# Kernel tuning notes

Hardware: AMD Instinct MI355X
Metric: run time of the kernel (lower is better)

Reference implementation:

```python
import jax, jax.numpy as jnp
import numpy as np

B, N, E, ATT, TT, IT = 32, 5000, 500, 50, 4, 24
TEMP = 0.5

def leaky(x):
    return jnp.where(x > 0, x, 0.1 * x)

def ln(x, g, b, eps=1e-5):
    m = jnp.mean(x, axis=-1, keepdims=True)
    v = jnp.mean((x - m) ** 2, axis=-1, keepdims=True)
    return (x - m) * jax.lax.rsqrt(v + eps) * g + b

def setup_inputs() -> dict:
    key = jax.random.key(0)
    ks = jax.random.split(key, 16)
    s = 0.05
    return {
        'positive_sample': jax.random.randint(ks[0], (B, 3), 0, N),
        'ent_text_emb': jax.random.normal(ks[1], (N, TT, 384), jnp.float32),
        'ent_img_emb': jax.random.normal(ks[2], (N, IT, 383), jnp.float32),
        'entity_embedding': jax.random.normal(ks[3], (N, E), jnp.float32) * s,
        'relation_embedding': jax.random.normal(ks[4], (N, E), jnp.float32) * s,
        'W_text': jax.random.normal(ks[5], (ATT, 384), jnp.float32) * s,
        'b_text': jnp.zeros((ATT,), jnp.float32),
        'W_img': jax.random.normal(ks[6], (ATT, 383), jnp.float32) * s,
        'b_img': jnp.zeros((ATT,), jnp.float32),
        'W_tproj': jax.random.normal(ks[7], (ATT, ATT * IT), jnp.float32) * s,
        'b_tproj': jnp.zeros((ATT,), jnp.float32),
        'W_iproj': jax.random.normal(ks[8], (ATT, ATT * TT), jnp.float32) * s,
        'b_iproj': jnp.zeros((ATT,), jnp.float32),
        'W_rel1': jax.random.normal(ks[9], (IT * TT, E), jnp.float32) * s,
        'b_rel1': jnp.zeros((IT * TT,), jnp.float32),
        'W_rel2': jax.random.normal(ks[10], (IT * TT, E), jnp.float32) * s,
        'b_rel2': jnp.zeros((IT * TT,), jnp.float32),
        'W1': jax.random.normal(ks[11], (100, 2 * E), jnp.float32) * s,
        'b1': jnp.zeros((100,), jnp.float32),
        'W3': jax.random.normal(ks[12], (E, 100), jnp.float32) * s,
        'b3': jnp.zeros((E,), jnp.float32),
        'ln_g': jnp.ones((ATT,), jnp.float32),
        'ln_b': jnp.zeros((ATT,), jnp.float32),
    }

def _cos_sim(X, p):
    # X [B,N,d], p [B,d]; denominators are detached as in the torch code
    num = jnp.einsum('bnd,bd->bn', X, p)
    den = jnp.linalg.norm(X, axis=2) * jnp.linalg.norm(p, axis=1)[:, None]
    return num / (jax.lax.stop_gradient(den) + 1e-10)

def reference(positive_sample, ent_text_emb, ent_img_emb, entity_embedding,
              relation_embedding, W_text, b_text, W_img, b_img, W_tproj, b_tproj,
              W_iproj, b_iproj, W_rel1, b_rel1, W_rel2, b_rel2, W1, b1, W3, b3,
              ln_g, ln_b):
    rel = relation_embedding[positive_sample[:, 1]]              # [B,E]
    text_emb = leaky(jnp.einsum('ntf,df->ntd', ent_text_emb, W_text) + b_text)  # [N,4,50]
    img_emb = leaky(jnp.einsum('nif,df->nid', ent_img_emb, W_img) + b_img)      # [N,24,50]
    cross = jnp.einsum('nid,ntd->nit', img_emb, text_emb)        # [N,24,4]

    # image branch: softmax over img tokens, plus relation-gated path
    img_att = jnp.einsum('nti,nid->ntd', jax.nn.softmax(cross.transpose(0, 2, 1), axis=2), img_emb)  # [N,4,50]
    rg_i = jax.nn.sigmoid(rel @ W_rel1.T + b_rel1).reshape(B, IT, TT)           # [B,24,4]
    gated_i = rg_i[:, None] * cross[None]                                        # [B,N,24,4]
    img_att_rg = jnp.einsum('bnit,nid->bntd', gated_i, img_emb)                  # [B,N,4,50]
    img_att_all = ln(img_att_rg, ln_g, ln_b) + ln(img_att, ln_g, ln_b)[None]
    img_att_all = img_att_all.reshape(B, N, TT * ATT) @ W_iproj.T + b_iproj      # [B,N,50]

    # text branch: softmax over text tokens, plus relation-gated path
    text_att = jnp.einsum('nit,ntd->nid', jax.nn.softmax(cross, axis=2), text_emb)  # [N,24,50]
    rg_t = jax.nn.sigmoid(rel @ W_rel2.T + b_rel2).reshape(B, IT, TT)
    gated_t = rg_t[:, None] * cross[None]                                        # [B,N,24,4]
    text_att_rg = jnp.einsum('bnit,ntd->bnid', gated_t, text_emb)                # [B,N,24,50]
    text_att_all = ln(text_att_rg, ln_g, ln_b) + ln(text_att, ln_g, ln_b)[None]
    text_att_all = text_att_all.reshape(B, N, IT * ATT) @ W_tproj.T + b_tproj    # [B,N,50]

    # structural gate on KGE entity embeddings (split W1 to avoid concat)
    h = leaky(entity_embedding @ W1[:, :E].T[None].squeeze(0).T.T  # placeholder removed below
              ) if False else None
    h = leaky((entity_embedding @ W1[:, :E].T)[None] + (rel @ W1[:, E:].T)[:, None] + b1)  # [B,N,100]
    gate = jax.nn.sigmoid(h @ W3.T + b3)                                         # [B,N,E]
    t_att = entity_embedding[None] * gate                                        # [B,N,E]

    pos_idx = positive_sample[:, 2]  # tail-batch
    bi = jnp.arange(B)
    pos_img = img_att_all[bi, pos_idx]    # [B,50]
    pos_text = text_att_all[bi, pos_idx]  # [B,50]
    pos_t = t_att[bi, pos_idx]            # [B,E]

    simil_img = _cos_sim(img_att_all, pos_img)
    simil_text = _cos_sim(text_att_all, pos_text)
    simil_t = _cos_sim(t_att, pos_t)

    out = (jax.nn.softmax(simil_t / TEMP, axis=1)
           + jax.nn.softmax(simil_img / TEMP, axis=1)
           + jax.nn.softmax(simil_text / TEMP, axis=1))
    return (out, simil_img, simil_text, simil_t)
```

## Files before the change

### kernel.cpp

```cpp
#include <hip/hip_runtime.h>
#include <math.h>

#define BB 32
#define NN 5000
#define EE 500
#define AT 50
#define TTT 4
#define ITT 24
#define FT 384
#define FI 383
#define KH 100
#define BN (BB*NN)

__device__ __forceinline__ float leaky(float x){ return x > 0.f ? x : 0.1f*x; }
__device__ __forceinline__ float sigm(float x){ return 1.f/(1.f+__expf(-x)); }

enum : size_t {
  O_WTT = 0,
  O_WIT = 19968,
  O_WIP = 39936,
  O_WTP = 50336,
  O_W1T = 112736,
  O_W3T = 162736,
  O_SIP = 212736,
  O_STP = 212944,
  O_CBI = 214192,
  O_CBT = 214244,
  O_RGI = 214296,
  O_RGT = 217368,
  O_RB  = 220440,
  O_A   = 223640,
  O_PT  = 723640,
  O_PTN = 739640,
  O_PIM = 739672,
  O_PIMN= 741336,
  O_PTX = 741368,
  O_PTXN= 743032,
  O_MR  = 743064,
  O_SR  = 743160,
  O_EMB = 743256,
};

__global__ void k_prep(const float* Wt, const float* Wi, const float* Wip, const float* Wtp,
                       const float* W1, const float* W3, const float* g, const float* lb,
                       const float* bip, const float* btp, float* ws){
  (void)W1;
  int id = blockIdx.x*256 + threadIdx.x;
  if (id < 19968){ int f=id/52, d=id%52; ws[O_WTT+id] = (d<50)? Wt[d*FT+f] : 0.f; return; }
  id -= 19968;
  if (id < 19968){ int f=id/52, d=id%52; ws[O_WIT+id] = (f<383 && d<50)? Wi[d*FI+f] : 0.f; return; }
  id -= 19968;
  if (id < 10400){
    int m=id>>2, c=id&3; int d=m%50, r=m/50; int q=r%13, t=r/13; int o=q*4+c;
    ws[O_WIP+id] = (o<50)? Wip[o*200+t*50+d]*g[o] : 0.f; return; }
  id -= 10400;
  if (id < 62400){
    int m=id>>2, c=id&3; int d=m%50, r=m/50; int q=r%13, i=r/13; int o=q*4+c;
    ws[O_WTP+id] = (o<50)? Wtp[o*1200+i*50+d]*g[o] : 0.f; return; }
  id -= 62400;
  if (id < 50000){ int k=id/500, e=id%500; ws[O_W3T+id] = W3[e*100+k]; return; }
  id -= 50000;
  if (id < 208){ int t=id/52, o=id%52; float s=0;
                 if (o<50) for(int d=0;d<50;d++) s += Wip[o*200+t*50+d]*g[d];
                 ws[O_SIP+id]=s; return; }
  id -= 208;
  if (id < 1248){ int i=id/52, o=id%52; float s=0;
                  if (o<50) for(int d=0;d<50;d++) s += Wtp[o*1200+i*50+d]*g[d];
                  ws[O_STP+id]=s; return; }
  id -= 1248;
  if (id < 52){ int o=id; float s=0;
                if (o<50){ for(int j=0;j<200;j++) s += lb[j%50]*Wip[o*200+j]; s=2.f*s+bip[o]; }
                ws[O_CBI+o]=s; return; }
  id -= 52;
  if (id < 52){ int o=id; float s=0;
                if (o<50){ for(int j=0;j<1200;j++) s += lb[j%50]*Wtp[o*1200+j]; s=2.f*s+btp[o]; }
                ws[O_CBT+o]=s; return; }
}

__global__ void k_rel(const int* ps, const float* rele, const float* Wr1, const float* br1,
                      const float* Wr2, const float* br2, const float* W1, float* ws){
  __shared__ float relL[EE];
  int b = blockIdx.x;
  int r = ps[b*3+1];
  for (int e=threadIdx.x; e<EE; e+=256) relL[e] = rele[(size_t)r*EE+e];
  __syncthreads();
  for (int j=threadIdx.x; j<292; j+=256){
    if (j<96){
      float a=br1[j]; const float* w=&Wr1[j*EE];
      for(int e=0;e<EE;e++) a+=relL[e]*w[e];
      ws[O_RGI+b*96+j]=sigm(a);
    } else if (j<192){
      int jj=j-96; float a=br2[jj]; const float* w=&Wr2[jj*EE];
      for(int e=0;e<EE;e++) a+=relL[e]*w[e];
      ws[O_RGT+b*96+jj]=sigm(a);
    } else {
      int k=j-192; float a=0; const float* w=&W1[k*1000+500];
      for(int e=0;e<EE;e++) a+=relL[e]*w[e];
      ws[O_RB+b*100+k]=a;
    }
  }
}

__global__ void k_A(const float* ent, const float* W1, float* ws){
  __shared__ __align__(16) float entL[8*EE];
  int n0 = blockIdx.x*8;
  for (int idx=threadIdx.x; idx<1000; idx+=256)
    *(float4*)&entL[idx*4] = *(const float4*)&ent[(size_t)n0*EE + idx*4];
  __syncthreads();
  for (int idx=threadIdx.x; idx<800; idx+=256){
    int k=idx>>3, rr=idx&7;
    const float4* el=(const float4*)&entL[rr*EE];
    const float4* wr=(const float4*)&W1[(size_t)k*1000];
    float s=0;
    for (int e4=0;e4<125;e4++){
      float4 a=el[e4], w=wr[e4];
      s += a.x*w.x + a.y*w.y + a.z*w.z + a.w*w.w;
    }
    ws[O_A + (size_t)k*NN + (n0+rr)] = s;
  }
}

__global__ void k_pos(const int* ps, const float* ent, const float* b1, const float* b3, float* ws){
  __shared__ float hL[KH];
  __shared__ float red[4];
  int b=blockIdx.x; int n=ps[b*3+2]; int tid=threadIdx.x;
  if (tid<KH) hL[tid] = leaky(ws[O_A+(size_t)tid*NN+n] + ws[O_RB+b*100+tid] + b1[tid]);
  __syncthreads();
  const float* w3t=&ws[O_W3T];
  float sq=0;
  for (int e=tid; e<EE; e+=256){
    float a=b3[e];
    for (int k=0;k<KH;k++) a += hL[k]*w3t[k*500+e];
    float gg=sigm(a); float ta=ent[(size_t)n*EE+e]*gg;
    ws[O_PT+b*500+e]=ta; sq+=ta*ta;
  }
  for (int off=1; off<64; off<<=1) sq += __shfl_xor(sq, off);
  if ((tid&63)==0) red[tid>>6]=sq;
  __syncthreads();
  if (tid==0) ws[O_PTN+b] = sqrtf(red[0]+red[1]+red[2]+red[3]);
}

__global__ __launch_bounds__(256) void k_emb2(const float* __restrict__ X,
                                              const float* __restrict__ Wp,
                                              const float* __restrict__ bias,
                                              float* __restrict__ emb,
                                              int R, int F, int rowsPerN, int rowOff,
                                              int xstride){
  __shared__ __align__(16) float part[4][64][52];
  int tid = threadIdx.x;
  int lane = tid & 63;
  int w = __builtin_amdgcn_readfirstlane(tid >> 6);
  int row = blockIdx.x*64 + lane;
  int fq = (F + 3) >> 2;
  int f0 = w*fq;
  int f1 = min(F, f0+fq);
  float4 acc[13];
  #pragma unroll
  for (int c=0;c<13;c++) acc[c]=make_float4(0,0,0,0);
  if (row < R){
    const float* xr = X + (size_t)row*xstride;
    for (int f=f0; f<f1; ++f){
      float x = xr[f];
      const float4* wr = (const float4*)(Wp + (size_t)f*52);
      #pragma unroll
      for (int c=0;c<13;++c){
        float4 wv=wr[c];
        acc[c].x+=x*wv.x; acc[c].y+=x*wv.y; acc[c].z+=x*wv.z; acc[c].w+=x*wv.w;
      }
    }
  }
  #pragma unroll
  for (int c=0;c<13;c++) *(float4*)&part[w][lane][c*4] = acc[c];
  __syncthreads();
  for (int g=tid; g<832; g+=256){
    int r = g/13, q = g-r*13;
    int row2 = blockIdx.x*64 + r;
    if (row2 < R){
      float4 s0 = *(const float4*)&part[0][r][q*4];
      float4 s1 = *(const float4*)&part[1][r][q*4];
      float4 s2 = *(const float4*)&part[2][r][q*4];
      float4 s3 = *(const float4*)&part[3][r][q*4];
      float4 v;
      v.x = leaky(s0.x+s1.x+s2.x+s3.x + bias[q*4+0]);
      v.y = leaky(s0.y+s1.y+s2.y+s3.y + bias[q*4+1]);
      v.z = (q<12)? leaky(s0.z+s1.z+s2.z+s3.z + bias[q*4+2]) : 0.f;
      v.w = (q<12)? leaky(s0.w+s1.w+s2.w+s3.w + bias[q*4+3]) : 0.f;
      int n = row2 / rowsPerN, rr = row2 % rowsPerN;
      *(float4*)&emb[(size_t)n*1456 + (size_t)(rowOff+rr)*52 + q*4] = v;
    }
  }
}

__global__ __launch_bounds__(256) void k_main(const int* ps, float* ws, float* out, int mode){
  __shared__ __align__(16) float teie[1456];
  __shared__ __align__(16) float Pm[120*52];
  __shared__ __align__(16) float Um[120*32];
  __shared__ __align__(16) float Gi[576];
  __shared__ __align__(16) float crs[96];
  __shared__ __align__(16) float aimg[96], atxt[96];
  __shared__ __align__(16) float part1[96], part2[96];
  __shared__ __align__(16) float aU[120];
  __shared__ float Gts[16], mimg[24], mtxt[4];
  __shared__ float muA1[4], muA2[24];
  __shared__ float accD1[32], accN1[32], accD2[32], accN2[32];

  int tid = threadIdx.x;
  int bstar = blockIdx.x;
  int n = mode ? ps[bstar*3+2] : blockIdx.x;

  const float* embn = &ws[O_EMB + (size_t)n*1456];
  for (int j=tid; j<364; j+=256) *(float4*)&teie[j*4] = *(const float4*)&embn[j*4];
  if (tid<32){ accD1[tid]=0.f; accN1[tid]=0.f; accD2[tid]=0.f; accN2[tid]=0.f; }
  __syncthreads();

  for (int it=tid; it<716; it+=256){
    if (it<576){
      int i=it/24, j=it%24;
      const float4* a=(const float4*)&teie[(4+i)*52];
      const float4* b=(const float4*)&teie[(4+j)*52];
      float s=0;
      #pragma unroll
      for(int d=0;d<13;d++){ float4 x=a[d], y=b[d]; s+=x.x*y.x+x.y*y.y+x.z*y.z+x.w*y.w; }
      Gi[it]=s;
    } else if (it<672){
      int c=it-576; int i=c>>2, t=c&3;
      const float4* a=(const float4*)&teie[(4+i)*52];
      const float4* b=(const float4*)&teie[t*52];
      float s=0;
      #pragma unroll
      for(int d=0;d<13;d++){ float4 x=a[d], y=b[d]; s+=x.x*y.x+x.y*y.y+x.z*y.z+x.w*y.w; }
      crs[c]=s;
    } else if (it<688){
      int c=it-672; int t=c>>2, u=c&3;
      const float4* a=(const float4*)&teie[t*52];
      const float4* b=(const float4*)&teie[u*52];
      float s=0;
      #pragma unroll
      for(int d=0;d<13;d++){ float4 x=a[d], y=b[d]; s+=x.x*y.x+x.y*y.y+x.z*y.z+x.w*y.w; }
      Gts[c]=s;
    } else if (it<712){
      int i=it-688;
      const float4* a=(const float4*)&teie[(4+i)*52];
      float s=0;
      #pragma unroll
      for(int d=0;d<13;d++){ float4 x=a[d]; s+=x.x+x.y+x.z+x.w; }
      mimg[i]=s*0.02f;
    } else {
      int t=it-712;
      const float4* a=(const float4*)&teie[t*52];
      float s=0;
      #pragma unroll
      for(int d=0;d<13;d++){ float4 x=a[d]; s+=x.x+x.y+x.z+x.w; }
      mtxt[t]=s*0.02f;
    }
  }
  __syncthreads();

  if (tid<4){
    int t=tid;
    float mx=-1e30f; for(int i=0;i<24;i++) mx=fmaxf(mx,crs[i*4+t]);
    float ex[24]; float s=0;
    for(int i=0;i<24;i++){ ex[i]=__expf(crs[i*4+t]-mx); s+=ex[i]; }
    float inv=1.f/s; float mu=0;
    for(int i=0;i<24;i++){ float a=ex[i]*inv; aimg[i*4+t]=a; mu+=a*mimg[i]; }
    muA1[t]=mu;
  } else if (tid>=64 && tid<88){
    int i=tid-64;
    float mx=-1e30f; for(int t=0;t<4;t++) mx=fmaxf(mx,crs[i*4+t]);
    float ex[4]; float s=0;
    for(int t=0;t<4;t++){ ex[t]=__expf(crs[i*4+t]-mx); s+=ex[t]; }
    float inv=1.f/s; float mu=0;
    for(int t=0;t<4;t++){ float a=ex[t]*inv; atxt[i*4+t]=a; mu+=a*mtxt[t]; }
    muA2[i]=mu;
  }
  __syncthreads();

  if (tid<208){
    int ig=tid&3, r=tid>>2, q=r%13, t=r/13;
    const float* wb = &ws[O_WIP + (size_t)(t*13+q)*200];
    const float* eb = &teie[(4+ig*6)*52];
    float4 acc[6];
    #pragma unroll
    for (int l=0;l<6;l++) acc[l]=make_float4(0,0,0,0);
    for (int dc=0; dc<12; ++dc){
      float e[6][4];
      #pragma unroll
      for (int l=0;l<6;l++){
        float4 v=*(const float4*)&eb[l*52+dc*4];
        e[l][0]=v.x; e[l][1]=v.y; e[l][2]=v.z; e[l][3]=v.w;
      }
      #pragma unroll
      for (int dd=0; dd<4; ++dd){
        float4 w=*(const float4*)&wb[(dc*4+dd)*4];
        #pragma unroll
        for (int l=0;l<6;l++){
          acc[l].x+=e[l][dd]*w.x; acc[l].y+=e[l][dd]*w.y;
          acc[l].z+=e[l][dd]*w.z; acc[l].w+=e[l][dd]*w.w;
        }
      }
    }
    #pragma unroll
    for (int d=48; d<50; ++d){
      float4 w=*(const float4*)&wb[d*4];
      #pragma unroll
      for (int l=0;l<6;l++){
        float ee=eb[l*52+d];
        acc[l].x+=ee*w.x; acc[l].y+=ee*w.y; acc[l].z+=ee*w.z; acc[l].w+=ee*w.w;
      }
    }
    #pragma unroll
    for (int l=0;l<6;l++) *(float4*)&Pm[(t*24+ig*6+l)*52 + q*4]=acc[l];
  } else {
    for (int c=tid-208; c<244; c+=48){
      if (c<96){
        int i=c>>2, t=c&3;
        float s=0; for(int j=0;j<24;j++) s+=Gi[i*24+j]*aimg[j*4+t];
        part1[c]=aimg[c]*s;
      } else if (c<192){
        int cc=c-96; int t=cc&3;
        float s=0; for(int u=0;u<4;u++) s+=Gts[t*4+u]*atxt[(cc&~3)+u];
        part2[cc]=atxt[cc]*s;
      } else {
        int j=c-192;
        *(float4*)&Pm[96*52+j*4] = *(const float4*)&ws[O_SIP+j*4];
      }
    }
  }
  __syncthreads();

  if (tid<128){
    int b=tid&31, t=tid>>5;
    float w1r[24];
    #pragma unroll
    for(int i=0;i<24;i++) w1r[i]=ws[O_RGI+b*96+i*4+t]*crs[i*4+t];
    float mu=0;
    #pragma unroll
    for(int i=0;i<24;i++) mu+=w1r[i]*mimg[i];
    float q=0;
    #pragma unroll
    for(int i=0;i<24;i++){
      const float4* gr=(const float4*)&Gi[i*24];
      float s=0;
      #pragma unroll
      for(int j4=0;j4<6;j4++){
        float4 g=gr[j4];
        s+=g.x*w1r[j4*4]+g.y*w1r[j4*4+1]+g.z*w1r[j4*4+2]+g.w*w1r[j4*4+3];
      }
      q+=w1r[i]*s;
    }
    float inv=rsqrtf(q*0.02f-mu*mu+1e-5f);
    #pragma unroll
    for(int i=0;i<24;i++) Um[(t*24+i)*32+b]=inv*w1r[i];
    Um[(96+t)*32+b]=-inv*mu;
  } else if (tid<228){
    int z=tid-128;
    int t=(z<96)? (z/24) : (z-96);
    float q=0; for(int i=0;i<24;i++) q+=part1[i*4+t];
    float inv=rsqrtf(q*0.02f-muA1[t]*muA1[t]+1e-5f);
    aU[z]=(z<96)? inv*aimg[(z%24)*4+t] : -inv*muA1[t];
  }
  __syncthreads();

  if (tid<104){
    int bg=tid/13, q=tid-bg*13;
    float4 a0=make_float4(0,0,0,0), a1=make_float4(0,0,0,0);
    float4 a2=make_float4(0,0,0,0), a3=make_float4(0,0,0,0);
    for (int z=0; z<100; ++z){
      float az=aU[z];
      float4 u=*(const float4*)&Um[z*32+bg*4];
      float4 p=*(const float4*)&Pm[z*52+q*4];
      float u0=u.x+az, u1=u.y+az, u2=u.z+az, u3=u.w+az;
      a0.x+=u0*p.x; a0.y+=u0*p.y; a0.z+=u0*p.z; a0.w+=u0*p.w;
      a1.x+=u1*p.x; a1.y+=u1*p.y; a1.z+=u1*p.z; a1.w+=u1*p.w;
      a2.x+=u2*p.x; a2.y+=u2*p.y; a2.z+=u2*p.z; a2.w+=u2*p.w;
      a3.x+=u3*p.x; a3.y+=u3*p.y; a3.z+=u3*p.z; a3.w+=u3*p.w;
    }
    float4 cb=*(const float4*)&ws[O_CBI+q*4];
    a0.x+=cb.x; a0.y+=cb.y; a0.z+=cb.z; a0.w+=cb.w;
    a1.x+=cb.x; a1.y+=cb.y; a1.z+=cb.z; a1.w+=cb.w;
    a2.x+=cb.x; a2.y+=cb.y; a2.z+=cb.z; a2.w+=cb.w;
    a3.x+=cb.x; a3.y+=cb.y; a3.z+=cb.z; a3.w+=cb.w;
    float n0=a0.x*a0.x+a0.y*a0.y+a0.z*a0.z+a0.w*a0.w;
    float n1=a1.x*a1.x+a1.y*a1.y+a1.z*a1.z+a1.w*a1.w;
    float n2=a2.x*a2.x+a2.y*a2.y+a2.z*a2.z+a2.w*a2.w;
    float n3=a3.x*a3.x+a3.y*a3.y+a3.z*a3.z+a3.w*a3.w;
    int b0=bg*4;
    if (!mode){
      const float* PV=&ws[O_PIM];
      float4 p0=*(const float4*)&PV[(b0+0)*52+q*4];
      float4 p1=*(const float4*)&PV[(b0+1)*52+q*4];
      float4 p2=*(const float4*)&PV[(b0+2)*52+q*4];
      float4 p3=*(const float4*)&PV[(b0+3)*52+q*4];
      atomicAdd(&accD1[b0+0], a0.x*p0.x+a0.y*p0.y+a0.z*p0.z+a0.w*p0.w);
      atomicAdd(&accD1[b0+1], a1.x*p1.x+a1.y*p1.y+a1.z*p1.z+a1.w*p1.w);
      atomicAdd(&accD1[b0+2], a2.x*p2.x+a2.y*p2.y+a2.z*p2.z+a2.w*p2.w);
      atomicAdd(&accD1[b0+3], a3.x*p3.x+a3.y*p3.y+a3.z*p3.z+a3.w*p3.w);
      atomicAdd(&accN1[b0+0],n0); atomicAdd(&accN1[b0+1],n1);
      atomicAdd(&accN1[b0+2],n2); atomicAdd(&accN1[b0+3],n3);
    } else {
      atomicAdd(&accN1[b0+0],n0); atomicAdd(&accN1[b0+1],n1);
      atomicAdd(&accN1[b0+2],n2); atomicAdd(&accN1[b0+3],n3);
      if ((bstar>>2)==bg){
        int bl=bstar&3;
        float4 sel = (bl==0)? a0 : (bl==1)? a1 : (bl==2)? a2 : a3;
        *(float4*)&ws[O_PIM+(size_t)bstar*52+q*4]=sel;
      }
    }
  }
  __syncthreads();

  if (!mode){
    if (tid<32)
      out[(size_t)BN + (size_t)tid*NN + n] = accD1[tid]/(sqrtf(accN1[tid])*ws[O_PIMN+tid]+1e-10f);
  } else {
    if (tid==0) ws[O_PIMN+bstar]=sqrtf(accN1[bstar]);
  }
  if (tid<156){
    int q=tid%13, i2=tid/13;
    const float* wbA = &ws[O_WTP + (size_t)((i2*2+0)*13+q)*200];
    const float* wbB = &ws[O_WTP + (size_t)((i2*2+1)*13+q)*200];
    float4 accA[4], accB[4];
    #pragma unroll
    for (int t=0;t<4;t++){ accA[t]=make_float4(0,0,0,0); accB[t]=make_float4(0,0,0,0); }
    for (int dc=0; dc<12; ++dc){
      float e[4][4];
      #pragma unroll
      for (int t=0;t<4;t++){
        float4 v=*(const float4*)&teie[t*52+dc*4];
        e[t][0]=v.x; e[t][1]=v.y; e[t][2]=v.z; e[t][3]=v.w;
      }
      #pragma unroll
      for (int dd=0; dd<4; ++dd){
        float4 wA=*(const float4*)&wbA[(dc*4+dd)*4];
        float4 wB=*(const float4*)&wbB[(dc*4+dd)*4];
        #pragma unroll
        for (int t=0;t<4;t++){
          accA[t].x+=e[t][dd]*wA.x; accA[t].y+=e[t][dd]*wA.y;
          accA[t].z+=e[t][dd]*wA.z; accA[t].w+=e[t][dd]*wA.w;
          accB[t].x+=e[t][dd]*wB.x; accB[t].y+=e[t][dd]*wB.y;
          accB[t].z+=e[t][dd]*wB.z; accB[t].w+=e[t][dd]*wB.w;
        }
      }
    }
    #pragma unroll
    for (int d=48; d<50; ++d){
      float4 wA=*(const float4*)&wbA[d*4];
      float4 wB=*(const float4*)&wbB[d*4];
      #pragma unroll
      for (int t=0;t<4;t++){
        float ee=teie[t*52+d];
        accA[t].x+=ee*wA.x; accA[t].y+=ee*wA.y; accA[t].z+=ee*wA.z; accA[t].w+=ee*wA.w;
        accB[t].x+=ee*wB.x; accB[t].y+=ee*wB.y; accB[t].z+=ee*wB.z; accB[t].w+=ee*wB.w;
      }
    }
    #pragma unroll
    for (int t=0;t<4;t++){
      *(float4*)&Pm[(t*24+i2*2+0)*52 + q*4]=accA[t];
      *(float4*)&Pm[(t*24+i2*2+1)*52 + q*4]=accB[t];
    }
  } else {
    for (int j=tid-156; j<312; j+=100)
      *(float4*)&Pm[96*52+j*4] = *(const float4*)&ws[O_STP+j*4];
  }
  __syncthreads();

  for (int it=tid; it<888; it+=256){
    if (it<768){
      int b=it&31, i=it>>5;
      float w2r[4];
      #pragma unroll
      for(int t=0;t<4;t++) w2r[t]=ws[O_RGT+b*96+i*4+t]*crs[i*4+t];
      float mu=0;
      #pragma unroll
      for(int t=0;t<4;t++) mu+=w2r[t]*mtxt[t];
      float q=0;
      #pragma unroll
      for(int t=0;t<4;t++){
        float s=0;
        #pragma unroll
        for(int u=0;u<4;u++) s+=Gts[t*4+u]*w2r[u];
        q+=w2r[t]*s;
      }
      float inv=rsqrtf(q*0.02f-mu*mu+1e-5f);
      #pragma unroll
      for(int t=0;t<4;t++) Um[(t*24+i)*32+b]=inv*w2r[t];
      Um[(96+i)*32+b]=-inv*mu;
    } else {
      int z=it-768;
      int i=(z<96)? (z%24) : (z-96);
      float q=0; for(int t=0;t<4;t++) q+=part2[i*4+t];
      float inv=rsqrtf(q*0.02f-muA2[i]*muA2[i]+1e-5f);
      aU[z]=(z<96)? inv*atxt[(z%24)*4+(z/24)] : -inv*muA2[i];
    }
  }
  __syncthreads();

  if (tid<104){
    int bg=tid/13, q=tid-bg*13;
    float4 a0=make_float4(0,0,0,0), a1=make_float4(0,0,0,0);
    float4 a2=make_float4(0,0,0,0), a3=make_float4(0,0,0,0);
    for (int z=0; z<120; ++z){
      float az=aU[z];
      float4 u=*(const float4*)&Um[z*32+bg*4];
      float4 p=*(const float4*)&Pm[z*52+q*4];
      float u0=u.x+az, u1=u.y+az, u2=u.z+az, u3=u.w+az;
      a0.x+=u0*p.x; a0.y+=u0*p.y; a0.z+=u0*p.z; a0.w+=u0*p.w;
      a1.x+=u1*p.x; a1.y+=u1*p.y; a1.z+=u1*p.z; a1.w+=u1*p.w;
      a2.x+=u2*p.x; a2.y+=u2*p.y; a2.z+=u2*p.z; a2.w+=u2*p.w;
      a3.x+=u3*p.x; a3.y+=u3*p.y; a3.z+=u3*p.z; a3.w+=u3*p.w;
    }
    float4 cb=*(const float4*)&ws[O_CBT+q*4];
    a0.x+=cb.x; a0.y+=cb.y; a0.z+=cb.z; a0.w+=cb.w;
    a1.x+=cb.x; a1.y+=cb.y; a1.z+=cb.z; a1.w+=cb.w;
    a2.x+=cb.x; a2.y+=cb.y; a2.z+=cb.z; a2.w+=cb.w;
    a3.x+=cb.x; a3.y+=cb.y; a3.z+=cb.z; a3.w+=cb.w;
    float n0=a0.x*a0.x+a0.y*a0.y+a0.z*a0.z+a0.w*a0.w;
    float n1=a1.x*a1.x+a1.y*a1.y+a1.z*a1.z+a1.w*a1.w;
    float n2=a2.x*a2.x+a2.y*a2.y+a2.z*a2.z+a2.w*a2.w;
    float n3=a3.x*a3.x+a3.y*a3.y+a3.z*a3.z+a3.w*a3.w;
    int b0=bg*4;
    if (!mode){
      const float* PV=&ws[O_PTX];
      float4 p0=*(const float4*)&PV[(b0+0)*52+q*4];
      float4 p1=*(const float4*)&PV[(b0+1)*52+q*4];
      float4 p2=*(const float4*)&PV[(b0+2)*52+q*4];
      float4 p3=*(const float4*)&PV[(b0+3)*52+q*4];
      atomicAdd(&accD2[b0+0], a0.x*p0.x+a0.y*p0.y+a0.z*p0.z+a0.w*p0.w);
      atomicAdd(&accD2[b0+1], a1.x*p1.x+a1.y*p1.y+a1.z*p1.z+a1.w*p1.w);
      atomicAdd(&accD2[b0+2], a2.x*p2.x+a2.y*p2.y+a2.z*p2.z+a2.w*p2.w);
      atomicAdd(&accD2[b0+3], a3.x*p3.x+a3.y*p3.y+a3.z*p3.z+a3.w*p3.w);
      atomicAdd(&accN2[b0+0],n0); atomicAdd(&accN2[b0+1],n1);
      atomicAdd(&accN2[b0+2],n2); atomicAdd(&accN2[b0+3],n3);
    } else {
      atomicAdd(&accN2[b0+0],n0); atomicAdd(&accN2[b0+1],n1);
      atomicAdd(&accN2[b0+2],n2); atomicAdd(&accN2[b0+3],n3);
      if ((bstar>>2)==bg){
        int bl=bstar&3;
        float4 sel = (bl==0)? a0 : (bl==1)? a1 : (bl==2)? a2 : a3;
        *(float4*)&ws[O_PTX+(size_t)bstar*52+q*4]=sel;
      }
    }
  }
  __syncthreads();

  if (!mode){
    if (tid<32)
      out[2*(size_t)BN + (size_t)tid*NN + n] = accD2[tid]/(sqrtf(accN2[tid])*ws[O_PTXN+tid]+1e-10f);
  } else {
    if (tid==0) ws[O_PTXN+bstar]=sqrtf(accN2[bstar]);
  }
}

__global__ __launch_bounds__(256) void k_gate(const float* ent, const float* b1, const float* b3,
                                              float* ws, float* out){
  __shared__ __align__(16) float hL[50*68];
  __shared__ __align__(16) float wc[50*128];
  __shared__ __align__(16) float PTb[512];
  __shared__ __align__(16) float b3L[512];
  __shared__ float rbL[KH];

  int tid = threadIdx.x;
  int b   = blockIdx.x & 31;
  int n0  = (blockIdx.x >> 5) * 64;

  for (int j=tid; j<512; j+=256){
    PTb[j] = (j<EE)? ws[O_PT + b*EE + j] : 0.f;
    b3L[j] = (j<EE)? b3[j] : 0.f;
  }
  if (tid < KH) rbL[tid] = ws[O_RB + b*KH + tid] + b1[tid];

  int ej = tid & 31;
  int ni = tid >> 5;

  float pn[8], ps[8];
  #pragma unroll
  for (int r=0;r<8;r++){ pn[r]=0.f; ps[r]=0.f; }

  for (int ec=0; ec<4; ++ec){
    int e0 = ec*128;
    float4 acc[8];
    #pragma unroll
    for (int r=0;r<8;r++) acc[r]=make_float4(0,0,0,0);

    for (int kh=0; kh<2; ++kh){
      __syncthreads();
      for (int idx=tid; idx<1600; idx+=256){
        int k = idx>>5, j4 = idx&31;
        int e = e0 + j4*4;
        float4 v = make_float4(0,0,0,0);
        if (e+3 < EE) v = *(const float4*)&ws[O_W3T + (size_t)(kh*50+k)*EE + e];
        *(float4*)&wc[k*128 + j4*4] = v;
      }
      for (int idx=tid; idx<3200; idx+=256){
        int k = idx>>6, nn = idx&63;
        int n = n0 + nn;
        float v = 0.f;
        if (n < NN) v = leaky(ws[O_A + (size_t)(kh*50+k)*NN + n] + rbL[kh*50+k]);
        hL[k*68 + nn] = v;
      }
      __syncthreads();

      const float4* wp = (const float4*)&wc[ej*4];
      const float4* hp = (const float4*)&hL[ni*8];
      #pragma unroll 2
      for (int k=0;k<50;k++){
        float4 w  = wp[k*32];
        float4 h0 = hp[k*17];
        float4 h1 = hp[k*17 + 1];
        acc[0].x+=h0.x*w.x; acc[0].y+=h0.x*w.y; acc[0].z+=h0.x*w.z; acc[0].w+=h0.x*w.w;
        acc[1].x+=h0.y*w.x; acc[1].y+=h0.y*w.y; acc[1].z+=h0.y*w.z; acc[1].w+=h0.y*w.w;
        acc[2].x+=h0.z*w.x; acc[2].y+=h0.z*w.y; acc[2].z+=h0.z*w.z; acc[2].w+=h0.z*w.w;
        acc[3].x+=h0.w*w.x; acc[3].y+=h0.w*w.y; acc[3].z+=h0.w*w.z; acc[3].w+=h0.w*w.w;
        acc[4].x+=h1.x*w.x; acc[4].y+=h1.x*w.y; acc[4].z+=h1.x*w.z; acc[4].w+=h1.x*w.w;
        acc[5].x+=h1.y*w.x; acc[5].y+=h1.y*w.y; acc[5].z+=h1.y*w.z; acc[5].w+=h1.y*w.w;
        acc[6].x+=h1.z*w.x; acc[6].y+=h1.z*w.y; acc[6].z+=h1.z*w.z; acc[6].w+=h1.z*w.w;
        acc[7].x+=h1.w*w.x; acc[7].y+=h1.w*w.y; acc[7].z+=h1.w*w.z; acc[7].w+=h1.w*w.w;
      }
    }

    {
      int ebase = e0 + ej*4;
      bool ev = (ebase + 3) < EE;
      float4 bb = *(const float4*)&b3L[ebase];
      float4 pt = *(const float4*)&PTb[ebase];
      #pragma unroll
      for (int r=0;r<8;r++){
        int n = n0 + ni*8 + r;
        float4 en = make_float4(0,0,0,0);
        if (ev && n < NN) en = *(const float4*)&ent[(size_t)n*EE + ebase];
        float t0 = en.x * sigm(acc[r].x + bb.x);
        float t1 = en.y * sigm(acc[r].y + bb.y);
        float t2 = en.z * sigm(acc[r].z + bb.z);
        float t3 = en.w * sigm(acc[r].w + bb.w);
        pn[r] += t0*pt.x + t1*pt.y + t2*pt.z + t3*pt.w;
        ps[r] += t0*t0 + t1*t1 + t2*t2 + t3*t3;
      }
    }
  }

  for (int off=1; off<32; off<<=1){
    #pragma unroll
    for (int r=0;r<8;r++){ pn[r]+=__shfl_xor(pn[r],off); ps[r]+=__shfl_xor(ps[r],off); }
  }
  if (ej==0){
    float ptn = ws[O_PTN+b];
    #pragma unroll
    for (int r=0;r<8;r++){
      int n = n0 + ni*8 + r;
      if (n < NN)
        out[3*(size_t)BN + (size_t)b*NN + n] = pn[r]/(sqrtf(ps[r])*ptn + 1e-10f);
    }
  }
}

__global__ void k_smax1(const float* out, float* ws){
  __shared__ float red[4];
  __shared__ float Msh;
  int a=blockIdx.x>>5, b=blockIdx.x&31, tid=threadIdx.x;
  const float* arr=&out[(size_t)(1+a)*BN + (size_t)b*NN];
  float mx=-1e30f;
  for (int i=tid;i<NN;i+=256) mx=fmaxf(mx,arr[i]);
  for (int off=1;off<64;off<<=1) mx=fmaxf(mx,__shfl_xor(mx,off));
  if ((tid&63)==0) red[tid>>6]=mx;
  __syncthreads();
  if (tid==0) Msh=fmaxf(fmaxf(red[0],red[1]),fmaxf(red[2],red[3]));
  __syncthreads();
  float M2=2.f*Msh;
  float s=0;
  for (int i=tid;i<NN;i+=256) s+=__expf(2.f*arr[i]-M2);
  for (int off=1;off<64;off<<=1) s+=__shfl_xor(s,off);
  if ((tid&63)==0) red[tid>>6]=s;
  __syncthreads();
  if (tid==0){ ws[O_MR+a*32+b]=M2; ws[O_SR+a*32+b]=red[0]+red[1]+red[2]+red[3]; }
}

__global__ void k_smax2(float* out, const float* ws){
  int t=blockIdx.x*256+threadIdx.x;
  if (t>=BN) return;
  int b=t/NN;
  float r=0;
  for (int a=0;a<3;a++)
    r += __expf(2.f*out[(size_t)(1+a)*BN+t]-ws[O_MR+a*32+b])/ws[O_SR+a*32+b];
  out[t]=r;
}

extern "C" void kernel_launch(void* const* d_in, const int* in_sizes, int n_in,
                              void* d_out, int out_size, void* d_ws, size_t ws_size,
                              hipStream_t stream){
  (void)in_sizes; (void)n_in; (void)out_size; (void)ws_size;
  const int*   ps  =(const int*)  d_in[0];
  const float* etg =(const float*)d_in[1];
  const float* eig =(const float*)d_in[2];
  const float* ent =(const float*)d_in[3];
  const float* rele=(const float*)d_in[4];
  const float* Wt  =(const float*)d_in[5];
  const float* btx =(const float*)d_in[6];
  const float* Wi  =(const float*)d_in[7];
  const float* bim =(const float*)d_in[8];
  const float* Wtp =(const float*)d_in[9];
  const float* btp =(const float*)d_in[10];
  const float* Wip =(const float*)d_in[11];
  const float* bip =(const float*)d_in[12];
  const float* Wr1 =(const float*)d_in[13];
  const float* br1 =(const float*)d_in[14];
  const float* Wr2 =(const float*)d_in[15];
  const float* br2 =(const float*)d_in[16];
  const float* W1  =(const float*)d_in[17];
  const float* b1  =(const float*)d_in[18];
  const float* W3  =(const float*)d_in[19];
  const float* b3  =(const float*)d_in[20];
  const float* lng =(const float*)d_in[21];
  const float* lnb =(const float*)d_in[22];
  float* ws =(float*)d_ws;
  float* out=(float*)d_out;

  k_prep <<<642,256,0,stream>>>(Wt,Wi,Wip,Wtp,W1,W3,lng,lnb,bip,btp,ws);
  k_rel  <<<32, 256,0,stream>>>(ps,rele,Wr1,br1,Wr2,br2,W1,ws);
  k_A    <<<625,256,0,stream>>>(ent,W1,ws);
  k_pos  <<<32, 256,0,stream>>>(ps,ent,b1,b3,ws);
  k_emb2 <<<313, 256,0,stream>>>(etg,&ws[O_WTT],btx,&ws[O_EMB],20000,FT,4,0,FT);
  k_emb2 <<<1875,256,0,stream>>>(eig,&ws[O_WIT],bim,&ws[O_EMB],120000,FI,24,4,FI);
  k_main <<<32,  256,0,stream>>>(ps,ws,out,1);
  k_main <<<5000,256,0,stream>>>(ps,ws,out,0);
  k_gate <<<32*79,256,0,stream>>>(ent,b1,b3,ws,out);
  k_smax1<<<96, 256,0,stream>>>(out,ws);
  k_smax2<<<625,256,0,stream>>>(out,ws);
}
```

Measured before the change: 1.457 ms.

## Fuse LN coefficient and projection stages using register accumulation and wave shuffles

The image and text attention stages used to write per-batch normalization coefficients into shared matrices (Um, aU), synchronize, and then run a separate small GEMM with shared-memory atomics for the dot products and norms. Now each thread computes its coefficients and multiplies them directly against the Pm rows, keeping a 13-float4 partial output in registers. Partials are combined with xor-shuffle reductions across 4 or 8 lanes, and one lane writes the cosine similarity. This removes several barriers, the shared atomics and some shared memory, at the cost of more registers per thread and redundant Pm reads across lanes.

```diff
diff --git a/kernel.cpp b/kernel.cpp
--- a/kernel.cpp
+++ b/kernel.cpp
@@ -194,15 +194,12 @@
 __global__ __launch_bounds__(256) void k_main(const int* ps, float* ws, float* out, int mode){
   __shared__ __align__(16) float teie[1456];
   __shared__ __align__(16) float Pm[120*52];
-  __shared__ __align__(16) float Um[120*32];
   __shared__ __align__(16) float Gi[576];
   __shared__ __align__(16) float crs[96];
   __shared__ __align__(16) float aimg[96], atxt[96];
   __shared__ __align__(16) float part1[96], part2[96];
-  __shared__ __align__(16) float aU[120];
   __shared__ float Gts[16], mimg[24], mtxt[4];
   __shared__ float muA1[4], muA2[24];
-  __shared__ float accD1[32], accN1[32], accD2[32], accN2[32];
 
   int tid = threadIdx.x;
   int bstar = blockIdx.x;
@@ -210,7 +207,6 @@
 
   const float* embn = &ws[O_EMB + (size_t)n*1456];
   for (int j=tid; j<364; j+=256) *(float4*)&teie[j*4] = *(const float4*)&embn[j*4];
-  if (tid<32){ accD1[tid]=0.f; accN1[tid]=0.f; accD2[tid]=0.f; accN2[tid]=0.f; }
   __syncthreads();
 
   for (int it=tid; it<716; it+=256){
@@ -328,8 +324,9 @@
   }
   __syncthreads();
 
-  if (tid<128){
-    int b=tid&31, t=tid>>5;
+  if (tid < 128){
+    int l = tid & 63, wv = tid >> 6;
+    int b = wv*16 + (l>>2), t = l&3;
     float w1r[24];
     #pragma unroll
     for(int i=0;i<24;i++) w1r[i]=ws[O_RGI+b*96+i*4+t]*crs[i*4+t];
@@ -349,72 +346,66 @@
       q+=w1r[i]*s;
     }
     float inv=rsqrtf(q*0.02f-mu*mu+1e-5f);
-    #pragma unroll
-    for(int i=0;i<24;i++) Um[(t*24+i)*32+b]=inv*w1r[i];
-    Um[(96+t)*32+b]=-inv*mu;
-  } else if (tid<228){
-    int z=tid-128;
-    int t=(z<96)? (z/24) : (z-96);
-    float q=0; for(int i=0;i<24;i++) q+=part1[i*4+t];
-    float inv=rsqrtf(q*0.02f-muA1[t]*muA1[t]+1e-5f);
-    aU[z]=(z<96)? inv*aimg[(z%24)*4+t] : -inv*muA1[t];
-  }
-  __syncthreads();
-
-  if (tid<104){
-    int bg=tid/13, q=tid-bg*13;
-    float4 a0=make_float4(0,0,0,0), a1=make_float4(0,0,0,0);
-    float4 a2=make_float4(0,0,0,0), a3=make_float4(0,0,0,0);
-    for (int z=0; z<100; ++z){
-      float az=aU[z];
-      float4 u=*(const float4*)&Um[z*32+bg*4];
-      float4 p=*(const float4*)&Pm[z*52+q*4];
-      float u0=u.x+az, u1=u.y+az, u2=u.z+az, u3=u.w+az;
-      a0.x+=u0*p.x; a0.y+=u0*p.y; a0.z+=u0*p.z; a0.w+=u0*p.w;
-      a1.x+=u1*p.x; a1.y+=u1*p.y; a1.z+=u1*p.z; a1.w+=u1*p.w;
-      a2.x+=u2*p.x; a2.y+=u2*p.y; a2.z+=u2*p.z; a2.w+=u2*p.w;
-      a3.x+=u3*p.x; a3.y+=u3*p.y; a3.z+=u3*p.z; a3.w+=u3*p.w;
-    }
-    float4 cb=*(const float4*)&ws[O_CBI+q*4];
-    a0.x+=cb.x; a0.y+=cb.y; a0.z+=cb.z; a0.w+=cb.w;
-    a1.x+=cb.x; a1.y+=cb.y; a1.z+=cb.z; a1.w+=cb.w;
-    a2.x+=cb.x; a2.y+=cb.y; a2.z+=cb.z; a2.w+=cb.w;
-    a3.x+=cb.x; a3.y+=cb.y; a3.z+=cb.z; a3.w+=cb.w;
-    float n0=a0.x*a0.x+a0.y*a0.y+a0.z*a0.z+a0.w*a0.w;
-    float n1=a1.x*a1.x+a1.y*a1.y+a1.z*a1.z+a1.w*a1.w;
-    float n2=a2.x*a2.x+a2.y*a2.y+a2.z*a2.z+a2.w*a2.w;
-    float n3=a3.x*a3.x+a3.y*a3.y+a3.z*a3.z+a3.w*a3.w;
-    int b0=bg*4;
-    if (!mode){
-      const float* PV=&ws[O_PIM];
-      float4 p0=*(const float4*)&PV[(b0+0)*52+q*4];
-      float4 p1=*(const float4*)&PV[(b0+1)*52+q*4];
-      float4 p2=*(const float4*)&PV[(b0+2)*52+q*4];
-      float4 p3=*(const float4*)&PV[(b0+3)*52+q*4];
-      atomicAdd(&accD1[b0+0], a0.x*p0.x+a0.y*p0.y+a0.z*p0.z+a0.w*p0.w);
-      atomicAdd(&accD1[b0+1], a1.x*p1.x+a1.y*p1.y+a1.z*p1.z+a1.w*p1.w);
-      atomicAdd(&accD1[b0+2], a2.x*p2.x+a2.y*p2.y+a2.z*p2.z+a2.w*p2.w);
-      atomicAdd(&accD1[b0+3], a3.x*p3.x+a3.y*p3.y+a3.z*p3.z+a3.w*p3.w);
-      atomicAdd(&accN1[b0+0],n0); atomicAdd(&accN1[b0+1],n1);
-      atomicAdd(&accN1[b0+2],n2); atomicAdd(&accN1[b0+3],n3);
-    } else {
-      atomicAdd(&accN1[b0+0],n0); atomicAdd(&accN1[b0+1],n1);
-      atomicAdd(&accN1[b0+2],n2); atomicAdd(&accN1[b0+3],n3);
-      if ((bstar>>2)==bg){
-        int bl=bstar&3;
-        float4 sel = (bl==0)? a0 : (bl==1)? a1 : (bl==2)? a2 : a3;
-        *(float4*)&ws[O_PIM+(size_t)bstar*52+q*4]=sel;
-      }
-    }
-  }
-  __syncthreads();
-
-  if (!mode){
-    if (tid<32)
-      out[(size_t)BN + (size_t)tid*NN + n] = accD1[tid]/(sqrtf(accN1[tid])*ws[O_PIMN+tid]+1e-10f);
-  } else {
-    if (tid==0) ws[O_PIMN+bstar]=sqrtf(accN1[bstar]);
-  }
+    float qa=0;
+    #pragma unroll
+    for(int i=0;i<24;i++) qa+=part1[i*4+t];
+    float invA=rsqrtf(qa*0.02f-muA1[t]*muA1[t]+1e-5f);
+
+    float4 res[13];
+    #pragma unroll
+    for (int c=0;c<13;c++) res[c]=make_float4(0,0,0,0);
+    for (int j=0;j<24;j++){
+      int i = j + t*6; if (i>=24) i-=24;
+      float c = inv*w1r[i] + invA*aimg[i*4+t];
+      const float4* pr=(const float4*)&Pm[(t*24+i)*52];
+      #pragma unroll
+      for (int cc=0;cc<13;cc++){
+        float4 p=pr[cc];
+        res[cc].x+=c*p.x; res[cc].y+=c*p.y; res[cc].z+=c*p.z; res[cc].w+=c*p.w;
+      }
+    }
+    {
+      float cS = -inv*mu - invA*muA1[t];
+      const float4* pr=(const float4*)&Pm[(96+t)*52];
+      #pragma unroll
+      for (int cc=0;cc<13;cc++){
+        float4 p=pr[cc];
+        res[cc].x+=cS*p.x; res[cc].y+=cS*p.y; res[cc].z+=cS*p.z; res[cc].w+=cS*p.w;
+      }
+    }
+    #pragma unroll
+    for (int cc=0;cc<13;cc++){
+      res[cc].x+=__shfl_xor(res[cc].x,1); res[cc].y+=__shfl_xor(res[cc].y,1);
+      res[cc].z+=__shfl_xor(res[cc].z,1); res[cc].w+=__shfl_xor(res[cc].w,1);
+      res[cc].x+=__shfl_xor(res[cc].x,2); res[cc].y+=__shfl_xor(res[cc].y,2);
+      res[cc].z+=__shfl_xor(res[cc].z,2); res[cc].w+=__shfl_xor(res[cc].w,2);
+    }
+    if (t==0){
+      float ni=0;
+      #pragma unroll
+      for (int cc=0;cc<13;cc++){
+        float4 cb=*(const float4*)&ws[O_CBI+cc*4];
+        res[cc].x+=cb.x; res[cc].y+=cb.y; res[cc].z+=cb.z; res[cc].w+=cb.w;
+        ni+=res[cc].x*res[cc].x+res[cc].y*res[cc].y+res[cc].z*res[cc].z+res[cc].w*res[cc].w;
+      }
+      if (!mode){
+        const float* pv=&ws[O_PIM+b*52];
+        float di=0;
+        #pragma unroll
+        for (int cc=0;cc<13;cc++){
+          float4 p=*(const float4*)&pv[cc*4];
+          di+=res[cc].x*p.x+res[cc].y*p.y+res[cc].z*p.z+res[cc].w*p.w;
+        }
+        out[(size_t)BN + (size_t)b*NN + n] = di/(sqrtf(ni)*ws[O_PIMN+b]+1e-10f);
+      } else if (b==bstar){
+        #pragma unroll
+        for (int cc=0;cc<13;cc++) *(float4*)&ws[O_PIM+(size_t)b*52+cc*4]=res[cc];
+        ws[O_PIMN+b]=sqrtf(ni);
+      }
+    }
+  }
+  __syncthreads();
+
   if (tid<156){
     int q=tid%13, i2=tid/13;
     const float* wbA = &ws[O_WTP + (size_t)((i2*2+0)*13+q)*200];
@@ -464,9 +455,15 @@
   }
   __syncthreads();
 
-  for (int it=tid; it<888; it+=256){
-    if (it<768){
-      int b=it&31, i=it>>5;
+  {
+    int l = tid & 63, wv = tid >> 6;
+    int b = wv*8 + (l>>3), ig = l&7;
+    float4 res[13];
+    #pragma unroll
+    for (int c=0;c<13;c++) res[c]=make_float4(0,0,0,0);
+    #pragma unroll
+    for (int jj=0;jj<3;jj++){
+      int i = ig*3+jj;
       float w2r[4];
       #pragma unroll
       for(int t=0;t<4;t++) w2r[t]=ws[O_RGT+b*96+i*4+t]*crs[i*4+t];
@@ -482,72 +479,60 @@
         q+=w2r[t]*s;
       }
       float inv=rsqrtf(q*0.02f-mu*mu+1e-5f);
-      #pragma unroll
-      for(int t=0;t<4;t++) Um[(t*24+i)*32+b]=inv*w2r[t];
-      Um[(96+i)*32+b]=-inv*mu;
-    } else {
-      int z=it-768;
-      int i=(z<96)? (z%24) : (z-96);
-      float q=0; for(int t=0;t<4;t++) q+=part2[i*4+t];
-      float inv=rsqrtf(q*0.02f-muA2[i]*muA2[i]+1e-5f);
-      aU[z]=(z<96)? inv*atxt[(z%24)*4+(z/24)] : -inv*muA2[i];
-    }
-  }
-  __syncthreads();
-
-  if (tid<104){
-    int bg=tid/13, q=tid-bg*13;
-    float4 a0=make_float4(0,0,0,0), a1=make_float4(0,0,0,0);
-    float4 a2=make_float4(0,0,0,0), a3=make_float4(0,0,0,0);
-    for (int z=0; z<120; ++z){
-      float az=aU[z];
-      float4 u=*(const float4*)&Um[z*32+bg*4];
-      float4 p=*(const float4*)&Pm[z*52+q*4];
-      float u0=u.x+az, u1=u.y+az, u2=u.z+az, u3=u.w+az;
-      a0.x+=u0*p.x; a0.y+=u0*p.y; a0.z+=u0*p.z; a0.w+=u0*p.w;
-      a1.x+=u1*p.x; a1.y+=u1*p.y; a1.z+=u1*p.z; a1.w+=u1*p.w;
-      a2.x+=u2*p.x; a2.y+=u2*p.y; a2.z+=u2*p.z; a2.w+=u2*p.w;
-      a3.x+=u3*p.x; a3.y+=u3*p.y; a3.z+=u3*p.z; a3.w+=u3*p.w;
-    }
-    float4 cb=*(const float4*)&ws[O_CBT+q*4];
-    a0.x+=cb.x; a0.y+=cb.y; a0.z+=cb.z; a0.w+=cb.w;
-    a1.x+=cb.x; a1.y+=cb.y; a1.z+=cb.z; a1.w+=cb.w;
-    a2.x+=cb.x; a2.y+=cb.y; a2.z+=cb.z; a2.w+=cb.w;
-    a3.x+=cb.x; a3.y+=cb.y; a3.z+=cb.z; a3.w+=cb.w;
-    float n0=a0.x*a0.x+a0.y*a0.y+a0.z*a0.z+a0.w*a0.w;
-    float n1=a1.x*a1.x+a1.y*a1.y+a1.z*a1.z+a1.w*a1.w;
-    float n2=a2.x*a2.x+a2.y*a2.y+a2.z*a2.z+a2.w*a2.w;
-    float n3=a3.x*a3.x+a3.y*a3.y+a3.z*a3.z+a3.w*a3.w;
-    int b0=bg*4;
-    if (!mode){
-      const float* PV=&ws[O_PTX];
-      float4 p0=*(const float4*)&PV[(b0+0)*52+q*4];
-      float4 p1=*(const float4*)&PV[(b0+1)*52+q*4];
-      float4 p2=*(const float4*)&PV[(b0+2)*52+q*4];
-      float4 p3=*(const float4*)&PV[(b0+3)*52+q*4];
-      atomicAdd(&accD2[b0+0], a0.x*p0.x+a0.y*p0.y+a0.z*p0.z+a0.w*p0.w);
-      atomicAdd(&accD2[b0+1], a1.x*p1.x+a1.y*p1.y+a1.z*p1.z+a1.w*p1.w);
-      atomicAdd(&accD2[b0+2], a2.x*p2.x+a2.y*p2.y+a2.z*p2.z+a2.w*p2.w);
-      atomicAdd(&accD2[b0+3], a3.x*p3.x+a3.y*p3.y+a3.z*p3.z+a3.w*p3.w);
-      atomicAdd(&accN2[b0+0],n0); atomicAdd(&accN2[b0+1],n1);
-      atomicAdd(&accN2[b0+2],n2); atomicAdd(&accN2[b0+3],n3);
-    } else {
-      atomicAdd(&accN2[b0+0],n0); atomicAdd(&accN2[b0+1],n1);
-      atomicAdd(&accN2[b0+2],n2); atomicAdd(&accN2[b0+3],n3);
-      if ((bstar>>2)==bg){
-        int bl=bstar&3;
-        float4 sel = (bl==0)? a0 : (bl==1)? a1 : (bl==2)? a2 : a3;
-        *(float4*)&ws[O_PTX+(size_t)bstar*52+q*4]=sel;
-      }
-    }
-  }
-  __syncthreads();
-
-  if (!mode){
-    if (tid<32)
-      out[2*(size_t)BN + (size_t)tid*NN + n] = accD2[tid]/(sqrtf(accN2[tid])*ws[O_PTXN+tid]+1e-10f);
-  } else {
-    if (tid==0) ws[O_PTXN+bstar]=sqrtf(accN2[bstar]);
+      float qa=part2[i*4+0]+part2[i*4+1]+part2[i*4+2]+part2[i*4+3];
+      float invA=rsqrtf(qa*0.02f-muA2[i]*muA2[i]+1e-5f);
+      #pragma unroll
+      for (int t=0;t<4;t++){
+        float c = inv*w2r[t] + invA*atxt[i*4+t];
+        const float4* pr=(const float4*)&Pm[(t*24+i)*52];
+        #pragma unroll
+        for (int cc=0;cc<13;cc++){
+          float4 p=pr[cc];
+          res[cc].x+=c*p.x; res[cc].y+=c*p.y; res[cc].z+=c*p.z; res[cc].w+=c*p.w;
+        }
+      }
+      {
+        float cS = -inv*mu - invA*muA2[i];
+        const float4* pr=(const float4*)&Pm[(96+i)*52];
+        #pragma unroll
+        for (int cc=0;cc<13;cc++){
+          float4 p=pr[cc];
+          res[cc].x+=cS*p.x; res[cc].y+=cS*p.y; res[cc].z+=cS*p.z; res[cc].w+=cS*p.w;
+        }
+      }
+    }
+    #pragma unroll
+    for (int cc=0;cc<13;cc++){
+      res[cc].x+=__shfl_xor(res[cc].x,1); res[cc].y+=__shfl_xor(res[cc].y,1);
+      res[cc].z+=__shfl_xor(res[cc].z,1); res[cc].w+=__shfl_xor(res[cc].w,1);
+      res[cc].x+=__shfl_xor(res[cc].x,2); res[cc].y+=__shfl_xor(res[cc].y,2);
+      res[cc].z+=__shfl_xor(res[cc].z,2); res[cc].w+=__shfl_xor(res[cc].w,2);
+      res[cc].x+=__shfl_xor(res[cc].x,4); res[cc].y+=__shfl_xor(res[cc].y,4);
+      res[cc].z+=__shfl_xor(res[cc].z,4); res[cc].w+=__shfl_xor(res[cc].w,4);
+    }
+    if (ig==0){
+      float ni=0;
+      #pragma unroll
+      for (int cc=0;cc<13;cc++){
+        float4 cb=*(const float4*)&ws[O_CBT+cc*4];
+        res[cc].x+=cb.x; res[cc].y+=cb.y; res[cc].z+=cb.z; res[cc].w+=cb.w;
+        ni+=res[cc].x*res[cc].x+res[cc].y*res[cc].y+res[cc].z*res[cc].z+res[cc].w*res[cc].w;
+      }
+      if (!mode){
+        const float* pv=&ws[O_PTX+b*52];
+        float di=0;
+        #pragma unroll
+        for (int cc=0;cc<13;cc++){
+          float4 p=*(const float4*)&pv[cc*4];
+          di+=res[cc].x*p.x+res[cc].y*p.y+res[cc].z*p.z+res[cc].w*p.w;
+        }
+        out[2*(size_t)BN + (size_t)b*NN + n] = di/(sqrtf(ni)*ws[O_PTXN+b]+1e-10f);
+      } else if (b==bstar){
+        #pragma unroll
+        for (int cc=0;cc<13;cc++) *(float4*)&ws[O_PTX+(size_t)b*52+cc*4]=res[cc];
+        ws[O_PTXN+b]=sqrtf(ni);
+      }
+    }
   }
 }
 
```

After: 1.754 ms. 20.4% more time.
